# Kernel tuning notes

Hardware: AMD Instinct MI355X
Metric: run time of the kernel (lower is better)

The kernel has to match this reference:

```python
import jax, jax.numpy as jnp
import numpy as np

ALPHA = 0.2          # LeakyReLU negative slope
N = 4096             # num nodes
E = 262144           # num edges (avg degree 64)
NFEAT = 512
NHID = 64
NHEAD = 8
NCLASS = 16
NEG_INF = -1e20


def setup_inputs() -> dict:
    key = jax.random.key(0)
    ks = jax.random.split(key, 8)
    features = jax.random.normal(ks[0], (N, NFEAT), dtype=jnp.float32)
    edge_list = jax.random.randint(ks[1], (2, E), 0, N, dtype=jnp.int64)
    # xavier-uniform-ish init scaled like gain=1.414
    W_heads = jax.random.normal(ks[2], (NHEAD, NFEAT, NHID), dtype=jnp.float32) * (1.414 / np.sqrt(NFEAT))
    a_heads = jax.random.normal(ks[3], (NHEAD, 2 * NHID, 1), dtype=jnp.float32) * 0.1
    b_heads = jnp.zeros((NHEAD, NHID), dtype=jnp.float32)
    W_out = jax.random.normal(ks[4], (NHEAD * NHID, NCLASS), dtype=jnp.float32) * (1.414 / np.sqrt(NHEAD * NHID))
    a_out = jax.random.normal(ks[5], (2 * NCLASS, 1), dtype=jnp.float32) * 0.1
    b_out = jnp.zeros((NCLASS,), dtype=jnp.float32)
    return {
        "features": features, "edge_list": edge_list,
        "W_heads": W_heads, "a_heads": a_heads, "b_heads": b_heads,
        "W_out": W_out, "a_out": a_out, "b_out": b_out,
    }


def _gatconv(x, src, tgt, W, a, b):
    # dropout layers are identity in eval mode
    h = x @ W                                             # [N, F_out]
    # edge scores: gather endpoints, concat, project, LeakyReLU
    a_input = jnp.concatenate([h[src], h[tgt]], axis=1)   # [E, 2*F_out]
    e = jax.nn.leaky_relu((a_input @ a)[:, 0], ALPHA)     # [E]
    n = h.shape[0]
    # dense NxN attention: -1e20 default, edge scores scattered in
    att = jnp.full((n, n), NEG_INF, dtype=h.dtype).at[src, tgt].set(e)
    att = jax.nn.softmax(att, axis=1)                     # rows w/o edges -> uniform (matches torch)
    return att @ h + b                                    # [N, F_out]


def reference(features, edge_list, W_heads, a_heads, b_heads, W_out, a_out, b_out):
    src, tgt = edge_list[0], edge_list[1]
    # multi-head GATConv, heads vmapped over stacked params -> [H, N, NHID]
    heads = jax.vmap(lambda W, a, b: _gatconv(features, src, tgt, W, a, b))(
        W_heads, a_heads, b_heads)
    # torch.cat over heads on dim=1 == transpose+reshape
    x = jnp.transpose(heads, (1, 0, 2)).reshape(N, NHEAD * NHID)
    x = jax.nn.elu(x)
    out = _gatconv(x, src, tgt, W_out, a_out, b_out)      # [N, NCLASS]
    return jax.nn.log_softmax(out, axis=1)
```

## Files before the change

kernel.cpp:

```cpp
#include <hip/hip_runtime.h>
#include <hip/hip_bf16.h>

#define NN 4096
#define NFEAT 512
#define NHID 64
#define NHEAD 8
#define NCLASS 16
#define CAP 192
#define LALPHA 0.2f

#define SZ2 (NHEAD*2*NHID)
#define SZ3 (NHEAD*NHID)
#define SZ4 (NFEAT*NCLASS)
#define SZ5 (2*NCLASS)
#define SZ6 (NCLASS)
#define NSMALL (SZ2+SZ3+SZ4+SZ5+SZ6)
#define NZERO (NN*NN/32 + NN + NHEAD*NHID + NCLASS)

typedef __attribute__((ext_vector_type(8))) short bf16x8;
typedef __attribute__((ext_vector_type(4))) float f32x4;
typedef __attribute__((ext_vector_type(8))) unsigned short u16x8;

__device__ __forceinline__ float b2f(unsigned short h) {
    return __uint_as_float(((unsigned int)h) << 16);
}
__device__ __forceinline__ unsigned short f2b(float f) {
    unsigned int u = __float_as_uint(f);
    unsigned int r = (u + 0x7fffu + ((u >> 16) & 1u)) >> 16;
    return (unsigned short)r;
}
__device__ __forceinline__ float waveMax(float v) {
#pragma unroll
    for (int m = 32; m >= 1; m >>= 1) v = fmaxf(v, __shfl_xor(v, m, 64));
    return v;
}
__device__ __forceinline__ float waveSum(float v) {
#pragma unroll
    for (int m = 32; m >= 1; m >>= 1) v += __shfl_xor(v, m, 64);
    return v;
}
__device__ __forceinline__ float lrelu(float e) {
    return e >= 0.f ? e : LALPHA * e;
}

__global__ void __launch_bounds__(256)
k_prep(const void* __restrict__ f, const void* __restrict__ Wh_,
       const void* __restrict__ ah_, const void* __restrict__ bh_,
       const void* __restrict__ Wo_, const void* __restrict__ ao_,
       const void* __restrict__ bo_, const int* __restrict__ e32,
       int E, int csb,
       unsigned short* __restrict__ featb,
       unsigned short* __restrict__ Wtb,
       float* __restrict__ smallf,
       unsigned int* __restrict__ bits) {
    __shared__ int sbf;
    int t = threadIdx.x;
    if (t < 64) {
        unsigned int w = ((const unsigned int*)f)[t];
        unsigned int lo = w & 0xffffu, e = (lo >> 7) & 0xffu;
        unsigned long long bal = __ballot(lo == 0u || (e >= 100u && e <= 140u));
        if (t == 0) sbf = (__popcll(bal) >= 40);
    }
    __syncthreads();
    bool bf = (sbf != 0);
    if (blockIdx.x < 128) {
        __shared__ float tile[64][33];
        int h = blockIdx.x >> 4, k0 = (blockIdx.x & 15) * 32;
        int n = t & 63, kh = t >> 6;
#pragma unroll
        for (int i = 0; i < 8; ++i) {
            int kk = kh * 8 + i;
            int si = (h << 15) + (k0 + kk) * NHID + n;
            float v = bf ? b2f(((const unsigned short*)Wh_)[si])
                         : ((const float*)Wh_)[si];
            tile[n][kk] = v;
        }
        __syncthreads();
        int n2 = t >> 2, kk0 = (t & 3) * 8;
        u16x8 o;
#pragma unroll
        for (int i = 0; i < 8; ++i) o[i] = f2b(tile[n2][kk0 + i]);
        *(u16x8*)&Wtb[(size_t)((h << 6) + n2) * NFEAT + k0 + kk0] = o;
    } else if ((int)blockIdx.x < 128 + csb) {
        __shared__ int s64f;
        if (t < 64) {
            unsigned long long bal = __ballot(e32[2 * t + 1] == 0);
            if (t == 0) s64f = (__popcll(bal) >= 48);
        }
        __syncthreads();
        int i = (blockIdx.x - 128) * 256 + t;
        if (i < E) {
            int s, tt;
            if (s64f) { s = e32[2 * i]; tt = e32[2 * (E + i)]; }
            else      { s = e32[i];     tt = e32[E + i]; }
            s &= (NN - 1); tt &= (NN - 1);
            unsigned int pos = (unsigned int)s * NN + (unsigned int)tt;
            atomicOr(&bits[pos >> 5], 1u << (pos & 31u));
        }
    } else {
        const int NF8 = NN * NFEAT / 8;
        int i = (blockIdx.x - 128 - csb) * 256 + t;
        int stride = (gridDim.x - 128 - csb) * 256;
        const int TOT = NF8 + NSMALL;
        for (; i < TOT; i += stride) {
            if (i < NF8) {
                if (bf) {
                    *(u16x8*)&featb[i * 8] = ((const u16x8*)f)[i];
                } else {
                    float4 lo = ((const float4*)f)[i * 2];
                    float4 hi = ((const float4*)f)[i * 2 + 1];
                    u16x8 o;
                    o[0] = f2b(lo.x); o[1] = f2b(lo.y); o[2] = f2b(lo.z); o[3] = f2b(lo.w);
                    o[4] = f2b(hi.x); o[5] = f2b(hi.y); o[6] = f2b(hi.z); o[7] = f2b(hi.w);
                    *(u16x8*)&featb[i * 8] = o;
                }
            } else {
                int r = i - NF8;
                const void* sp; int off;
                if (r < SZ2)                        { sp = ah_; off = r; }
                else if (r < SZ2 + SZ3)             { sp = bh_; off = r - SZ2; }
                else if (r < SZ2 + SZ3 + SZ4)       { sp = Wo_; off = r - SZ2 - SZ3; }
                else if (r < SZ2 + SZ3 + SZ4 + SZ5) { sp = ao_; off = r - SZ2 - SZ3 - SZ4; }
                else                                { sp = bo_; off = r - SZ2 - SZ3 - SZ4 - SZ5; }
                smallf[r] = bf ? b2f(((const unsigned short*)sp)[off])
                               : ((const float*)sp)[off];
            }
        }
    }
}

__global__ void __launch_bounds__(256)
k_gemm_ext(const unsigned short* __restrict__ Ab,
           const unsigned short* __restrict__ Wtb,
           const float* __restrict__ ah,
           unsigned short* __restrict__ Hb,
           float* __restrict__ s1, float* __restrict__ s2,
           float* __restrict__ cm1,
           const unsigned int* __restrict__ bits,
           int* __restrict__ deg, int* __restrict__ csr) {
    int t = threadIdx.x;
    if (blockIdx.x >= 256) {
        int wid = t >> 6, lane = t & 63;
        int n = (blockIdx.x - 256) * 4 + wid;
        uint2 w = *(const uint2*)&bits[n * 128 + lane * 2];
        int c = __popc(w.x) + __popc(w.y);
        int incl = c;
#pragma unroll
        for (int off = 1; off < 64; off <<= 1) {
            int u = __shfl_up(incl, off, 64);
            if (lane >= off) incl += u;
        }
        int excl = incl - c;
        int total = __shfl(incl, 63, 64);
        if (lane == 0) deg[n] = total;
        int base = n * CAP;
        int tbase = lane * 64;
        unsigned int x = w.x;
        while (x) {
            int b = __ffs(x) - 1; x &= x - 1;
            if (excl < CAP) csr[base + excl] = tbase + b;
            ++excl;
        }
        unsigned int y = w.y;
        while (y) {
            int b = __ffs(y) - 1; y &= y - 1;
            if (excl < CAP) csr[base + excl] = tbase + 32 + b;
            ++excl;
        }
        return;
    }
    __shared__ float cms[64];
    if (t < 64) cms[t] = 0.f;
    __syncthreads();
    int w = t >> 6, l = t & 63;
    int quad = l >> 4, l16 = l & 15;
    int h = blockIdx.x >> 5;
    int m0 = (blockIdx.x & 31) * 128 + w * 32;
    f32x4 acc[2][4] = {};
    const unsigned short* a0p = Ab + (size_t)(m0 + l16) * NFEAT + quad * 8;
    const unsigned short* a1p = a0p + 16 * NFEAT;
    const unsigned short* bp  = Wtb + ((size_t)h << 15) + (size_t)l16 * NFEAT + quad * 8;
#pragma unroll 4
    for (int k0 = 0; k0 < NFEAT; k0 += 32) {
        bf16x8 a0 = *(const bf16x8*)(a0p + k0);
        bf16x8 a1 = *(const bf16x8*)(a1p + k0);
#pragma unroll
        for (int nt = 0; nt < 4; ++nt) {
            bf16x8 b = *(const bf16x8*)(bp + (size_t)nt * 16 * NFEAT + k0);
            acc[0][nt] = __builtin_amdgcn_mfma_f32_16x16x32_bf16(a0, b, acc[0][nt], 0, 0, 0);
            acc[1][nt] = __builtin_amdgcn_mfma_f32_16x16x32_bf16(a1, b, acc[1][nt], 0, 0, 0);
        }
    }
    const float* av = ah + h * 2 * NHID;
    float p1[2][4] = {}, p2[2][4] = {};
#pragma unroll
    for (int rh = 0; rh < 2; ++rh) {
#pragma unroll
        for (int nt = 0; nt < 4; ++nt) {
            int col = nt * 16 + l16;
            float av1 = av[col], av2 = av[NHID + col];
            float csum = 0.f;
#pragma unroll
            for (int r = 0; r < 4; ++r) {
                float v = acc[rh][nt][r];
                int row = m0 + rh * 16 + quad * 4 + r;
                Hb[(((size_t)h << 12) + row) * NHID + col] = f2b(v);
                p1[rh][r] += v * av1;
                p2[rh][r] += v * av2;
                csum += v;
            }
            atomicAdd(&cms[col], csum);
        }
    }
#pragma unroll
    for (int m = 8; m >= 1; m >>= 1)
#pragma unroll
        for (int rh = 0; rh < 2; ++rh)
#pragma unroll
            for (int r = 0; r < 4; ++r) {
                p1[rh][r] += __shfl_xor(p1[rh][r], m, 64);
                p2[rh][r] += __shfl_xor(p2[rh][r], m, 64);
            }
    if (l16 == 0) {
#pragma unroll
        for (int rh = 0; rh < 2; ++rh)
#pragma unroll
            for (int r = 0; r < 4; ++r) {
                int row = m0 + rh * 16 + quad * 4 + r;
                s1[(h << 12) + row] = p1[rh][r];
                s2[(h << 12) + row] = p2[rh][r];
            }
    }
    __syncthreads();
    if (t < 64) atomicAdd(&cm1[h * NHID + t], cms[t]);
}

__global__ void __launch_bounds__(256)
k_attn1(const int* __restrict__ deg, const int* __restrict__ csr,
        const float* __restrict__ s1, const float* __restrict__ s2,
        const unsigned short* __restrict__ Hb, const float* __restrict__ bh,
        const float* __restrict__ cm1, float* __restrict__ X) {
    __shared__ float2 wts[4][CAP];
    int wid = threadIdx.x >> 6, lane = threadIdx.x & 63;
    int idx = blockIdx.x * 4 + wid;
    int n = idx & (NN - 1), h = idx >> 12;
    int e8 = lane & 7, g = lane >> 3;
    int d = min(deg[n], CAP);
    float acc[8] = {};
    float den = 1.f;
    if (d > 0) {
        float s1n = s1[idx];
        const float* s2h = s2 + ((size_t)h << 12);
        const int* row = csr + (size_t)n * CAP;
        int t0 = (lane < d)       ? (row[lane]       & (NN - 1)) : 0;
        int t1 = (lane + 64 < d)  ? (row[lane + 64]  & (NN - 1)) : 0;
        int t2 = (lane + 128 < d) ? (row[lane + 128] & (NN - 1)) : 0;
        float e0 = (lane < d)       ? lrelu(s1n + s2h[t0]) : -1e30f;
        float e1 = (lane + 64 < d)  ? lrelu(s1n + s2h[t1]) : -1e30f;
        float e2 = (lane + 128 < d) ? lrelu(s1n + s2h[t2]) : -1e30f;
        float m = waveMax(fmaxf(e0, fmaxf(e1, e2)));
        float w0 = (lane < d)       ? __expf(e0 - m) : 0.f;
        float w1 = (lane + 64 < d)  ? __expf(e1 - m) : 0.f;
        float w2 = (lane + 128 < d) ? __expf(e2 - m) : 0.f;
        den = waveSum(w0 + w1 + w2);
        wts[wid][lane]       = make_float2(w0, __int_as_float(t0 << 6));
        wts[wid][lane + 64]  = make_float2(w1, __int_as_float(t1 << 6));
        wts[wid][lane + 128] = make_float2(w2, __int_as_float(t2 << 6));
        const unsigned short* Hp = Hb + (((size_t)h << 12) * NHID) + e8 * 8;
#pragma unroll 2
        for (int j = g; j < d; j += 8) {
            float2 p = wts[wid][j];
            u16x8 v = *(const u16x8*)(Hp + __float_as_int(p.y));
#pragma unroll
            for (int i = 0; i < 8; ++i) acc[i] += p.x * b2f(v[i]);
        }
#pragma unroll
        for (int m2 = 8; m2 <= 32; m2 <<= 1)
#pragma unroll
            for (int i = 0; i < 8; ++i) acc[i] += __shfl_xor(acc[i], m2, 64);
    }
    if (lane < 8) {
        float o[8];
        if (d == 0) {
            const float* c = cm1 + h * NHID + lane * 8;
#pragma unroll
            for (int i = 0; i < 8; ++i) o[i] = c[i] * (1.0f / NN);
        } else {
            float rden = 1.0f / den;
#pragma unroll
            for (int i = 0; i < 8; ++i) o[i] = acc[i] * rden;
        }
        const float* b8p = bh + h * NHID + lane * 8;
#pragma unroll
        for (int i = 0; i < 8; ++i) {
            float v = o[i] + b8p[i];
            o[i] = v > 0.f ? v : __expf(v) - 1.f;
        }
        float* xp = &X[(size_t)n * NFEAT + h * NHID + lane * 8];
        *(float4*)xp       = make_float4(o[0], o[1], o[2], o[3]);
        *(float4*)(xp + 4) = make_float4(o[4], o[5], o[6], o[7]);
    }
}

__global__ void __launch_bounds__(256)
k_gemm2f(const float* __restrict__ X, const float* __restrict__ Wo,
         const float* __restrict__ ao, float* __restrict__ out2,
         float* __restrict__ s1o, float* __restrict__ s2o,
         float* __restrict__ cm2) {
    __shared__ float cms[16];
    int t = threadIdx.x;
    if (t < 16) cms[t] = 0.f;
    __syncthreads();
    int wid = t >> 6, lane = t & 63;
    int n = blockIdx.x * 4 + wid;
    int c = lane & 15, sub = lane >> 4;
    const float* xr = X + (size_t)n * NFEAT + sub * 128;
    const float* wr = Wo + sub * 128 * NCLASS + c;
    float acc = 0.f;
#pragma unroll 8
    for (int kk = 0; kk < 128; ++kk) acc += xr[kk] * wr[kk * NCLASS];
    acc += __shfl_xor(acc, 16, 64);
    acc += __shfl_xor(acc, 32, 64);
    if (lane < 16) out2[n * NCLASS + c] = acc;
    float r1 = acc * ao[c], r2 = acc * ao[NCLASS + c];
#pragma unroll
    for (int m = 8; m >= 1; m >>= 1) {
        r1 += __shfl_xor(r1, m, 16);
        r2 += __shfl_xor(r2, m, 16);
    }
    if (lane == 0) { s1o[n] = r1; s2o[n] = r2; }
    if (lane < 16) atomicAdd(&cms[c], acc);
    __syncthreads();
    if (t < 16) atomicAdd(&cm2[t], cms[t]);
}

__global__ void __launch_bounds__(256)
k_attn2(const int* __restrict__ deg, const int* __restrict__ csr,
        const float* __restrict__ s1o, const float* __restrict__ s2o,
        const float* __restrict__ out2, const float* __restrict__ bo,
        const float* __restrict__ cm2, float* __restrict__ outp) {
    __shared__ float2 wts[4][CAP];
    __shared__ float o2s[4][16];
    int wid = threadIdx.x >> 6, lane = threadIdx.x & 63;
    int n = blockIdx.x * 4 + wid;
    int c = lane & 15;
    int d = min(deg[n], CAP);
    float val;
    if (d == 0) {
        val = cm2[c] * (1.0f / NN);
    } else {
        float s1n = s1o[n];
        const int* row = csr + (size_t)n * CAP;
        int t0 = (lane < d)       ? (row[lane]       & (NN - 1)) : 0;
        int t1 = (lane + 64 < d)  ? (row[lane + 64]  & (NN - 1)) : 0;
        int t2 = (lane + 128 < d) ? (row[lane + 128] & (NN - 1)) : 0;
        float e0 = (lane < d)       ? lrelu(s1n + s2o[t0]) : -1e30f;
        float e1 = (lane + 64 < d)  ? lrelu(s1n + s2o[t1]) : -1e30f;
        float e2 = (lane + 128 < d) ? lrelu(s1n + s2o[t2]) : -1e30f;
        float m = waveMax(fmaxf(e0, fmaxf(e1, e2)));
        float w0 = (lane < d)       ? __expf(e0 - m) : 0.f;
        float w1 = (lane + 64 < d)  ? __expf(e1 - m) : 0.f;
        float w2 = (lane + 128 < d) ? __expf(e2 - m) : 0.f;
        float den = waveSum(w0 + w1 + w2);
        wts[wid][lane]       = make_float2(w0, __int_as_float(t0 << 4));
        wts[wid][lane + 64]  = make_float2(w1, __int_as_float(t1 << 4));
        wts[wid][lane + 128] = make_float2(w2, __int_as_float(t2 << 4));
        int g2 = lane >> 2, q = lane & 3;
        float a4[4] = {};
        for (int j = g2; j < d; j += 16) {
            float2 p = wts[wid][j];
            float4 v = *(const float4*)(out2 + __float_as_int(p.y) + q * 4);
            a4[0] += p.x * v.x; a4[1] += p.x * v.y;
            a4[2] += p.x * v.z; a4[3] += p.x * v.w;
        }
#pragma unroll
        for (int m2 = 4; m2 <= 32; m2 <<= 1)
#pragma unroll
            for (int i = 0; i < 4; ++i) a4[i] += __shfl_xor(a4[i], m2, 64);
        if (lane < 4)
            *(float4*)&o2s[wid][lane * 4] = make_float4(a4[0], a4[1], a4[2], a4[3]);
        val = o2s[wid][c] / den;
    }
    val += bo[c];
    float mx = val;
#pragma unroll
    for (int m = 8; m >= 1; m >>= 1) mx = fmaxf(mx, __shfl_xor(mx, m, 16));
    float se = __expf(val - mx);
#pragma unroll
    for (int m = 8; m >= 1; m >>= 1) se += __shfl_xor(se, m, 16);
    float res = val - mx - __logf(se);
    if (lane < 16) outp[n * NCLASS + lane] = res;
}

extern "C" void kernel_launch(void* const* d_in, const int* in_sizes, int n_in,
                              void* d_out, int out_size, void* d_ws, size_t ws_size,
                              hipStream_t stream) {
    const void* features = d_in[0];
    const int*  edges    = (const int*)d_in[1];
    const void* W_heads  = d_in[2];
    const void* a_heads  = d_in[3];
    const void* b_heads  = d_in[4];
    const void* W_out    = d_in[5];
    const void* a_out    = d_in[6];
    const void* b_out    = d_in[7];
    int E = in_sizes[1] / 2;

    unsigned int* bits = (unsigned int*)d_ws;
    int*   deg  = (int*)(bits + (NN * NN / 32));
    float* cm1  = (float*)(deg + NN);
    float* cm2  = cm1 + NHEAD * NHID;
    int*   csr  = (int*)(cm2 + NCLASS);
    float* s1   = (float*)(csr + NN * CAP);
    float* s2   = s1 + NHEAD * NN;
    float* X    = s2 + NHEAD * NN;
    float* out2 = X + (size_t)NN * NFEAT;
    float* s1o  = out2 + NN * NCLASS;
    float* s2o  = s1o + NN;
    unsigned short* Hb    = (unsigned short*)(s2o + NN);
    unsigned short* featb = Hb + (size_t)NHEAD * NN * NHID;
    unsigned short* Wtb   = featb + (size_t)NN * NFEAT;
    float* smallf = (float*)(Wtb + NHEAD * NHID * NFEAT);
    float* ahf = smallf;
    float* bhf = ahf + SZ2;
    float* Wof = bhf + SZ3;
    float* aof = Wof + SZ4;
    float* bof = aof + SZ5;
    float* outp = (float*)d_out;

    int csb = (E + 255) / 256;
    hipMemsetAsync(d_ws, 0, (size_t)NZERO * 4, stream);
    hipLaunchKernelGGL(k_prep, dim3(128 + csb + 896), dim3(256), 0, stream,
                       features, W_heads, a_heads, b_heads, W_out, a_out, b_out,
                       edges, E, csb, featb, Wtb, smallf, bits);
    hipLaunchKernelGGL(k_gemm_ext, dim3(256 + NN / 4), dim3(256), 0, stream,
                       featb, Wtb, ahf, Hb, s1, s2, cm1, bits, deg, csr);
    hipLaunchKernelGGL(k_attn1, dim3(NN * NHEAD / 4), dim3(256), 0, stream,
                       deg, csr, s1, s2, Hb, bhf, cm1, X);
    hipLaunchKernelGGL(k_gemm2f, dim3(NN / 4), dim3(256), 0, stream,
                       X, Wof, aof, out2, s1o, s2o, cm2);
    hipLaunchKernelGGL(k_attn2, dim3(NN / 4), dim3(256), 0, stream,
                       deg, csr, s1o, s2o, out2, bof, cm2, outp);
}
```

Measured before the change: 163.7 us.

## Fuse layer-1 attention with output projection using node-major H layout

Changes the Hb layout from head-major to node-major, so one wave can gather all 8 heads' 64-wide rows for a neighbor in a single contiguous 1KB read. The layer-1 attention now processes all heads of a node in one wave and writes the ELU output into shared memory. The second-layer projection (the former k_gemm2f) runs in the same kernel, which removes the X round-trip through global memory and one launch. In exchange, the grid shrinks from 8192 to 1024 blocks, each block uses more shared memory, and the softmax loops over edges per head serially, lowering parallelism per node.

Measured after the change: 147.3 us. -10.0%, faster.

```diff
diff --git a/kernel.cpp b/kernel.cpp
--- a/kernel.cpp
+++ b/kernel.cpp
@@ -204,7 +204,7 @@
             for (int r = 0; r < 4; ++r) {
                 float v = acc[rh][nt][r];
                 int row = m0 + rh * 16 + quad * 4 + r;
-                Hb[(((size_t)h << 12) + row) * NHID + col] = f2b(v);
+                Hb[((size_t)row << 9) + (h << 6) + col] = f2b(v);
                 p1[rh][r] += v * av1;
                 p2[rh][r] += v * av2;
                 csum += v;
@@ -236,102 +236,109 @@
 }
 
 __global__ void __launch_bounds__(256)
-k_attn1(const int* __restrict__ deg, const int* __restrict__ csr,
-        const float* __restrict__ s1, const float* __restrict__ s2,
-        const unsigned short* __restrict__ Hb, const float* __restrict__ bh,
-        const float* __restrict__ cm1, float* __restrict__ X) {
-    __shared__ float2 wts[4][CAP];
-    int wid = threadIdx.x >> 6, lane = threadIdx.x & 63;
-    int idx = blockIdx.x * 4 + wid;
-    int n = idx & (NN - 1), h = idx >> 12;
-    int e8 = lane & 7, g = lane >> 3;
-    int d = min(deg[n], CAP);
-    float acc[8] = {};
-    float den = 1.f;
-    if (d > 0) {
-        float s1n = s1[idx];
-        const float* s2h = s2 + ((size_t)h << 12);
-        const int* row = csr + (size_t)n * CAP;
-        int t0 = (lane < d)       ? (row[lane]       & (NN - 1)) : 0;
-        int t1 = (lane + 64 < d)  ? (row[lane + 64]  & (NN - 1)) : 0;
-        int t2 = (lane + 128 < d) ? (row[lane + 128] & (NN - 1)) : 0;
-        float e0 = (lane < d)       ? lrelu(s1n + s2h[t0]) : -1e30f;
-        float e1 = (lane + 64 < d)  ? lrelu(s1n + s2h[t1]) : -1e30f;
-        float e2 = (lane + 128 < d) ? lrelu(s1n + s2h[t2]) : -1e30f;
-        float m = waveMax(fmaxf(e0, fmaxf(e1, e2)));
-        float w0 = (lane < d)       ? __expf(e0 - m) : 0.f;
-        float w1 = (lane + 64 < d)  ? __expf(e1 - m) : 0.f;
-        float w2 = (lane + 128 < d) ? __expf(e2 - m) : 0.f;
-        den = waveSum(w0 + w1 + w2);
-        wts[wid][lane]       = make_float2(w0, __int_as_float(t0 << 6));
-        wts[wid][lane + 64]  = make_float2(w1, __int_as_float(t1 << 6));
-        wts[wid][lane + 128] = make_float2(w2, __int_as_float(t2 << 6));
-        const unsigned short* Hp = Hb + (((size_t)h << 12) * NHID) + e8 * 8;
-#pragma unroll 2
-        for (int j = g; j < d; j += 8) {
-            float2 p = wts[wid][j];
-            u16x8 v = *(const u16x8*)(Hp + __float_as_int(p.y));
-#pragma unroll
-            for (int i = 0; i < 8; ++i) acc[i] += p.x * b2f(v[i]);
-        }
-#pragma unroll
-        for (int m2 = 8; m2 <= 32; m2 <<= 1)
-#pragma unroll
-            for (int i = 0; i < 8; ++i) acc[i] += __shfl_xor(acc[i], m2, 64);
-    }
-    if (lane < 8) {
-        float o[8];
-        if (d == 0) {
-            const float* c = cm1 + h * NHID + lane * 8;
-#pragma unroll
-            for (int i = 0; i < 8; ++i) o[i] = c[i] * (1.0f / NN);
-        } else {
-            float rden = 1.0f / den;
-#pragma unroll
-            for (int i = 0; i < 8; ++i) o[i] = acc[i] * rden;
-        }
-        const float* b8p = bh + h * NHID + lane * 8;
-#pragma unroll
-        for (int i = 0; i < 8; ++i) {
-            float v = o[i] + b8p[i];
-            o[i] = v > 0.f ? v : __expf(v) - 1.f;
-        }
-        float* xp = &X[(size_t)n * NFEAT + h * NHID + lane * 8];
-        *(float4*)xp       = make_float4(o[0], o[1], o[2], o[3]);
-        *(float4*)(xp + 4) = make_float4(o[4], o[5], o[6], o[7]);
-    }
-}
-
-__global__ void __launch_bounds__(256)
-k_gemm2f(const float* __restrict__ X, const float* __restrict__ Wo,
-         const float* __restrict__ ao, float* __restrict__ out2,
-         float* __restrict__ s1o, float* __restrict__ s2o,
-         float* __restrict__ cm2) {
-    __shared__ float cms[16];
+k_attn1f(const int* __restrict__ deg, const int* __restrict__ csr,
+         const float* __restrict__ s1, const float* __restrict__ s2,
+         const unsigned short* __restrict__ Hb,
+         const float* __restrict__ bh, const float* __restrict__ cm1,
+         const float* __restrict__ Wo, const float* __restrict__ ao,
+         float* __restrict__ out2, float* __restrict__ s1o,
+         float* __restrict__ s2o, float* __restrict__ cm2) {
+    __shared__ float sW[4][CAP * 8];
+    __shared__ int   sT[4][CAP];
+    __shared__ float xr[4][NFEAT];
+    __shared__ float cms[NCLASS];
     int t = threadIdx.x;
-    if (t < 16) cms[t] = 0.f;
+    if (t < NCLASS) cms[t] = 0.f;
     __syncthreads();
     int wid = t >> 6, lane = t & 63;
     int n = blockIdx.x * 4 + wid;
+    int h = lane >> 3, jslot = lane & 7;
+    int d = min(deg[n], CAP);
+    float acc[8] = {};
+    float rden = 1.f;
+    if (d > 0) {
+        const int* row = csr + (size_t)n * CAP;
+        const float* s2h = s2 + ((size_t)h << 12);
+        float s1n = s1[(h << 12) + n];
+        float mx = -1e30f;
+        for (int jb = 0; jb < d; jb += 8) {
+            int j = jb + jslot;
+            int tt = (j < d) ? (row[j] & (NN - 1)) : 0;
+            float e = (j < d) ? lrelu(s1n + s2h[tt]) : -1e30f;
+            sW[wid][(j << 3) + h] = e;
+            if (h == 0) sT[wid][j] = tt;
+            mx = fmaxf(mx, e);
+        }
+        mx = fmaxf(mx, __shfl_xor(mx, 1, 64));
+        mx = fmaxf(mx, __shfl_xor(mx, 2, 64));
+        mx = fmaxf(mx, __shfl_xor(mx, 4, 64));
+        float den = 0.f;
+        for (int jb = 0; jb < d; jb += 8) {
+            int j = jb + jslot;
+            float e = sW[wid][(j << 3) + h];
+            float w = __expf(e - mx);
+            sW[wid][(j << 3) + h] = w;
+            den += w;
+        }
+        den += __shfl_xor(den, 1, 64);
+        den += __shfl_xor(den, 2, 64);
+        den += __shfl_xor(den, 4, 64);
+        rden = 1.f / den;
+        const unsigned short* Hp = Hb + lane * 8;
+        int j = 0;
+#pragma unroll 2
+        for (; j + 2 <= d; j += 2) {
+            int t0 = sT[wid][j], t1 = sT[wid][j + 1];
+            float w0 = sW[wid][(j << 3) + h];
+            float w1 = sW[wid][((j + 1) << 3) + h];
+            u16x8 v0 = *(const u16x8*)(Hp + ((size_t)t0 << 9));
+            u16x8 v1 = *(const u16x8*)(Hp + ((size_t)t1 << 9));
+#pragma unroll
+            for (int i = 0; i < 8; ++i)
+                acc[i] += w0 * b2f(v0[i]) + w1 * b2f(v1[i]);
+        }
+        if (j < d) {
+            int t0 = sT[wid][j];
+            float w0 = sW[wid][(j << 3) + h];
+            u16x8 v0 = *(const u16x8*)(Hp + ((size_t)t0 << 9));
+#pragma unroll
+            for (int i = 0; i < 8; ++i) acc[i] += w0 * b2f(v0[i]);
+        }
+    }
+    float o[8];
+    if (d == 0) {
+#pragma unroll
+        for (int i = 0; i < 8; ++i) o[i] = cm1[lane * 8 + i] * (1.0f / NN);
+    } else {
+#pragma unroll
+        for (int i = 0; i < 8; ++i) o[i] = acc[i] * rden;
+    }
+#pragma unroll
+    for (int i = 0; i < 8; ++i) {
+        float v = o[i] + bh[lane * 8 + i];
+        o[i] = v > 0.f ? v : __expf(v) - 1.f;
+    }
+    *(float4*)&xr[wid][lane * 8]     = make_float4(o[0], o[1], o[2], o[3]);
+    *(float4*)&xr[wid][lane * 8 + 4] = make_float4(o[4], o[5], o[6], o[7]);
     int c = lane & 15, sub = lane >> 4;
-    const float* xr = X + (size_t)n * NFEAT + sub * 128;
-    const float* wr = Wo + sub * 128 * NCLASS + c;
-    float acc = 0.f;
+    const float* xp = &xr[wid][sub * 128];
+    const float* wp = Wo + sub * 128 * NCLASS + c;
+    float a2 = 0.f;
 #pragma unroll 8
-    for (int kk = 0; kk < 128; ++kk) acc += xr[kk] * wr[kk * NCLASS];
-    acc += __shfl_xor(acc, 16, 64);
-    acc += __shfl_xor(acc, 32, 64);
-    if (lane < 16) out2[n * NCLASS + c] = acc;
-    float r1 = acc * ao[c], r2 = acc * ao[NCLASS + c];
+    for (int kk = 0; kk < 128; ++kk) a2 += xp[kk] * wp[kk * NCLASS];
+    a2 += __shfl_xor(a2, 16, 64);
+    a2 += __shfl_xor(a2, 32, 64);
+    if (lane < 16) out2[n * NCLASS + c] = a2;
+    float r1 = a2 * ao[c], r2 = a2 * ao[NCLASS + c];
 #pragma unroll
     for (int m = 8; m >= 1; m >>= 1) {
         r1 += __shfl_xor(r1, m, 16);
         r2 += __shfl_xor(r2, m, 16);
     }
     if (lane == 0) { s1o[n] = r1; s2o[n] = r2; }
-    if (lane < 16) atomicAdd(&cms[c], acc);
+    if (lane < 16) atomicAdd(&cms[c], a2);
     __syncthreads();
-    if (t < 16) atomicAdd(&cm2[t], cms[t]);
+    if (t < NCLASS) atomicAdd(&cm2[t], cms[t]);
 }
 
 __global__ void __launch_bounds__(256)
@@ -412,8 +419,7 @@
     int*   csr  = (int*)(cm2 + NCLASS);
     float* s1   = (float*)(csr + NN * CAP);
     float* s2   = s1 + NHEAD * NN;
-    float* X    = s2 + NHEAD * NN;
-    float* out2 = X + (size_t)NN * NFEAT;
+    float* out2 = s2 + NHEAD * NN;
     float* s1o  = out2 + NN * NCLASS;
     float* s2o  = s1o + NN;
     unsigned short* Hb    = (unsigned short*)(s2o + NN);
@@ -434,10 +440,8 @@
                        edges, E, csb, featb, Wtb, smallf, bits);
     hipLaunchKernelGGL(k_gemm_ext, dim3(256 + NN / 4), dim3(256), 0, stream,
                        featb, Wtb, ahf, Hb, s1, s2, cm1, bits, deg, csr);
-    hipLaunchKernelGGL(k_attn1, dim3(NN * NHEAD / 4), dim3(256), 0, stream,
-                       deg, csr, s1, s2, Hb, bhf, cm1, X);
-    hipLaunchKernelGGL(k_gemm2f, dim3(NN / 4), dim3(256), 0, stream,
-                       X, Wof, aof, out2, s1o, s2o, cm2);
+    hipLaunchKernelGGL(k_attn1f, dim3(NN / 4), dim3(256), 0, stream,
+                       deg, csr, s1, s2, Hb, bhf, cm1, Wof, aof, out2, s1o, s2o, cm2);
     hipLaunchKernelGGL(k_attn2, dim3(NN / 4), dim3(256), 0, stream,
                        deg, csr, s1o, s2o, out2, bof, cm2, outp);
 }
```
